# Performance work log

Measured on AMD Instinct MI355X. Metric: run time of the kernel, lower is better.

Reference implementation:

```python
import jax, jax.numpy as jnp
import numpy as np

N_NODES = 200000
N_EDGES = 6400000
D_FEAT = 128
N_CLASSES = 40


def setup_inputs() -> dict:
    key = jax.random.key(0)
    ks = jax.random.split(key, 10)
    s_in = 1.0 / np.sqrt(D_FEAT)
    return {
        "x": jax.random.normal(ks[0], (N_NODES, D_FEAT), dtype=jnp.float32),
        "edge_index": jax.random.randint(ks[1], (2, N_EDGES), 0, N_NODES, dtype=jnp.int64),
        "W0": jax.random.normal(ks[2], (D_FEAT, D_FEAT), dtype=jnp.float32) * s_in,
        "b0": jnp.zeros((D_FEAT,), dtype=jnp.float32),
        "W1": jax.random.normal(ks[3], (D_FEAT, D_FEAT), dtype=jnp.float32) * s_in,
        "b1": jnp.zeros((D_FEAT,), dtype=jnp.float32),
        "W2": jax.random.normal(ks[4], (D_FEAT, D_FEAT), dtype=jnp.float32) * s_in,
        "b2": jnp.zeros((D_FEAT,), dtype=jnp.float32),
        "W3": jax.random.normal(ks[5], (D_FEAT, N_CLASSES), dtype=jnp.float32) * s_in,
        "b3": jnp.zeros((N_CLASSES,), dtype=jnp.float32),
    }


def _silu(h):
    return h * jax.nn.sigmoid(h)


def reference(x, edge_index, W0, b0, W1, b1, W2, b2, W3, b3):
    # PyG ChebConv with K=1: out = Tx_0 @ weight[0] + bias, Tx_0 = x.
    # edge_index feeds the scaled-Laplacian norm, which is unused when K == 1.
    del edge_index
    h = _silu(x @ W0 + b0)            # [N, D] ChebConv + SiLU
    h = _silu(h @ W1 + b1)            # [N, D]
    h = _silu(h @ W2 + b2)            # [N, D]
    logits = h @ W3 + b3              # [N, C]
    return jax.nn.log_softmax(logits, axis=1)
```

## Files before the change

kernel.cpp:

```cpp
#include <hip/hip_runtime.h>

#define NN 200000
#define NW 12
#define NBLK 256
#define NT 12500
#define WSTRIDE (NBLK * NW)

typedef __attribute__((ext_vector_type(8))) short bf16x8;
typedef __attribute__((ext_vector_type(4))) float f32x4;
typedef __attribute__((ext_vector_type(4))) unsigned int u32x4;

static __device__ __forceinline__ short f2bf(float f) {
    unsigned u = __builtin_bit_cast(unsigned, f);
    u += 0x7fffu + ((u >> 16) & 1u);
    return (short)(u >> 16);
}

static __device__ __forceinline__ unsigned pk2(float a, float b) {
    unsigned ua = __builtin_bit_cast(unsigned, a) + 0x8000u;
    unsigned ub = __builtin_bit_cast(unsigned, b) + 0x8000u;
    return __builtin_amdgcn_perm(ub, ua, 0x07060302u);
}

static __device__ __forceinline__ int swz(int r, int k) {
    return (r << 7) + (((k >> 3) ^ (r & 15)) << 3) + (k & 7);
}

__global__ void prep_weights_k(const float* __restrict__ W0, const float* __restrict__ W1,
                               const float* __restrict__ W2, const float* __restrict__ W3,
                               short* __restrict__ wt) {
    int e = blockIdx.x * 256 + threadIdx.x;
    if (e < 49152) {
        int l = e >> 14;
        int i = e & 16383;
        int n = i >> 7, k = i & 127;
        const float* W = (l == 0) ? W0 : ((l == 1) ? W1 : W2);
        wt[e] = f2bf(W[(k << 7) + n]);
    } else if (e < 55296) {
        int i = e - 49152;
        int n = i >> 7, k = i & 127;
        wt[e] = (n < 40) ? f2bf(W3[k * 40 + n]) : (short)0;
    }
}

__global__ __launch_bounds__(768) __attribute__((amdgpu_waves_per_eu(3, 3)))
void mlp_fused_k(const float* __restrict__ x, const short* __restrict__ wt,
                 const float* __restrict__ b0, const float* __restrict__ b1,
                 const float* __restrict__ b2, const float* __restrict__ b3,
                 float* __restrict__ out) {
    __shared__ __align__(16) short sW[55296];
    __shared__ __align__(16) short sA[NW][2048];
    __shared__ __align__(16) float sB[384];

    const int tid  = (int)threadIdx.x;
    const int lane = tid & 63;
    const int wv   = tid >> 6;
    const int m    = lane & 15;
    const int quad = lane >> 4;
    short* sAw = &sA[wv][0];

    {
        const u32x4* src = (const u32x4*)wt;
        #pragma unroll
        for (int i = 0; i < 9; ++i) {
            int q = tid + i * 768;
            int R = q >> 4, c = q & 15;
            *(u32x4*)&sW[(R << 7) + ((c ^ (R & 15)) << 3)] = src[q];
        }
        if (tid < 384)
            sB[tid] = (tid < 128) ? b0[tid] : (tid < 256) ? b1[tid - 128] : b2[tid - 256];
    }
    __syncthreads();

    const bool val2 = (m < 8);
    const float b3v0 = b3[m], b3v1 = b3[16 + m], b3v2 = val2 ? b3[32 + m] : 0.f;

    f32x4 acc[8];
    auto zacc = [&]() {
        #pragma unroll
        for (int ct = 0; ct < 8; ++ct)
            #pragma unroll
            for (int r = 0; r < 4; ++r) acc[ct][r] = 0.f;
    };

    auto epilogue = [&](int lyr) {
        float bb[8];
        #pragma unroll
        for (int ct = 0; ct < 8; ++ct) bb[ct] = sB[(lyr << 7) + (ct << 4) + m];
        #pragma unroll
        for (int ct = 0; ct < 8; ++ct)
            #pragma unroll
            for (int r = 0; r < 4; ++r) {
                float v = acc[ct][r] + bb[ct];
                float h = v * __builtin_amdgcn_rcpf(1.f + __expf(-v));
                int rl = (quad << 2) + r;
                unsigned u = __builtin_bit_cast(unsigned, h) + 0x8000u;
                sAw[swz(rl, (ct << 4) + m)] = (short)(u >> 16);
            }
    };

    auto dense = [&](int lbase) {
        zacc();
        __builtin_amdgcn_s_setprio(1);
        #pragma unroll
        for (int ks = 0; ks < 4; ++ks) {
            int kk = (ks << 5) + (quad << 3);
            bf16x8 a0 = *(const bf16x8*)&sAw[swz(m, kk)];
            #pragma unroll
            for (int ct = 0; ct < 8; ++ct) {
                bf16x8 b = *(const bf16x8*)&sW[lbase + swz((ct << 4) + m, kk)];
                acc[ct] = __builtin_amdgcn_mfma_f32_16x16x32_bf16(a0, b, acc[ct], 0, 0, 0);
            }
        }
        __builtin_amdgcn_s_setprio(0);
    };

    int t = (int)blockIdx.x * NW + wv;
    f32x4 raw[8];
    {
        const f32x4* p = (const f32x4*)(x + ((long)(t * 16 + m) << 7)) + quad * 2;
        #pragma unroll
        for (int ks = 0; ks < 4; ++ks) { raw[ks * 2] = p[ks * 8]; raw[ks * 2 + 1] = p[ks * 8 + 1]; }
    }

    while (true) {
        u32x4 xp[4];
        #pragma unroll
        for (int ks = 0; ks < 4; ++ks) {
            f32x4 va = raw[ks * 2], vb = raw[ks * 2 + 1];
            u32x4 ua;
            ua[0] = pk2(va[0], va[1]); ua[1] = pk2(va[2], va[3]);
            ua[2] = pk2(vb[0], vb[1]); ua[3] = pk2(vb[2], vb[3]);
            xp[ks] = ua;
        }

        zacc();
        __builtin_amdgcn_s_setprio(1);
        #pragma unroll
        for (int ks = 0; ks < 4; ++ks) {
            bf16x8 a0 = __builtin_bit_cast(bf16x8, xp[ks]);
            int kk = (ks << 5) + (quad << 3);
            #pragma unroll
            for (int ct = 0; ct < 8; ++ct) {
                bf16x8 b = *(const bf16x8*)&sW[swz((ct << 4) + m, kk)];
                acc[ct] = __builtin_amdgcn_mfma_f32_16x16x32_bf16(a0, b, acc[ct], 0, 0, 0);
            }
        }
        __builtin_amdgcn_s_setprio(0);
        epilogue(0);
        dense(16384);
        epilogue(1);
        dense(32768);
        epilogue(2);

        int tn = t + WSTRIDE;
        bool has = tn < NT;
        if (has) {
            const f32x4* p = (const f32x4*)(x + ((long)(tn * 16 + m) << 7)) + quad * 2;
            #pragma unroll
            for (int ks = 0; ks < 4; ++ks) { raw[ks * 2] = p[ks * 8]; raw[ks * 2 + 1] = p[ks * 8 + 1]; }
        }

        f32x4 c3[3];
        #pragma unroll
        for (int ct = 0; ct < 3; ++ct)
            #pragma unroll
            for (int r = 0; r < 4; ++r) c3[ct][r] = 0.f;
        __builtin_amdgcn_s_setprio(1);
        #pragma unroll
        for (int ks = 0; ks < 4; ++ks) {
            int kk = (ks << 5) + (quad << 3);
            bf16x8 a0 = *(const bf16x8*)&sAw[swz(m, kk)];
            #pragma unroll
            for (int ct = 0; ct < 3; ++ct) {
                bf16x8 b = *(const bf16x8*)&sW[49152 + swz((ct << 4) + m, kk)];
                c3[ct] = __builtin_amdgcn_mfma_f32_16x16x32_bf16(a0, b, c3[ct], 0, 0, 0);
            }
        }
        __builtin_amdgcn_s_setprio(0);
        #pragma unroll
        for (int r = 0; r < 4; ++r) {
            float v0 = c3[0][r] + b3v0;
            float v1 = c3[1][r] + b3v1;
            float v2 = c3[2][r] + b3v2;
            float mx = fmaxf(v0, v1);
            mx = val2 ? fmaxf(mx, v2) : mx;
            #pragma unroll
            for (int s = 1; s < 16; s <<= 1)
                mx = fmaxf(mx, __shfl_xor(mx, s, 64));
            float sm = __expf(v0 - mx) + __expf(v1 - mx) + (val2 ? __expf(v2 - mx) : 0.f);
            #pragma unroll
            for (int s = 1; s < 16; s <<= 1)
                sm += __shfl_xor(sm, s, 64);
            float L = mx + __logf(sm);
            int grow = t * 16 + (quad << 2) + r;
            float* orow = out + (long)grow * 40;
            orow[m]      = v0 - L;
            orow[16 + m] = v1 - L;
            if (val2) orow[32 + m] = v2 - L;
        }

        if (!has) break;
        t = tn;
    }
}

extern "C" void kernel_launch(void* const* d_in, const int* in_sizes, int n_in,
                              void* d_out, int out_size, void* d_ws, size_t ws_size,
                              hipStream_t stream) {
    const float* x   = (const float*)d_in[0];
    const float* W0  = (const float*)d_in[2];
    const float* bb0 = (const float*)d_in[3];
    const float* W1  = (const float*)d_in[4];
    const float* bb1 = (const float*)d_in[5];
    const float* W2  = (const float*)d_in[6];
    const float* bb2 = (const float*)d_in[7];
    const float* W3  = (const float*)d_in[8];
    const float* bb3 = (const float*)d_in[9];
    short* wt  = (short*)d_ws;
    float* out = (float*)d_out;

    hipLaunchKernelGGL(prep_weights_k, dim3(216), dim3(256), 0, stream, W0, W1, W2, W3, wt);
    hipLaunchKernelGGL(mlp_fused_k, dim3(NBLK), dim3(768), 0, stream,
                       x, wt, bb0, bb1, bb2, bb3, out);
}
```

Baseline: 216.6 us.

## Pack biases into padded weight rows and raise waves per block to thirteen

```diff
diff --git a/kernel.cpp b/kernel.cpp
--- a/kernel.cpp
+++ b/kernel.cpp
@@ -1,7 +1,7 @@
 #include <hip/hip_runtime.h>
 
 #define NN 200000
-#define NW 12
+#define NW 13
 #define NBLK 256
 #define NT 12500
 #define WSTRIDE (NBLK * NW)
@@ -28,7 +28,8 @@
 
 __global__ void prep_weights_k(const float* __restrict__ W0, const float* __restrict__ W1,
                                const float* __restrict__ W2, const float* __restrict__ W3,
-                               short* __restrict__ wt) {
+                               const float* __restrict__ b0, const float* __restrict__ b1,
+                               const float* __restrict__ b2, short* __restrict__ wt) {
     int e = blockIdx.x * 256 + threadIdx.x;
     if (e < 49152) {
         int l = e >> 14;
@@ -39,18 +40,27 @@
     } else if (e < 55296) {
         int i = e - 49152;
         int n = i >> 7, k = i & 127;
-        wt[e] = (n < 40) ? f2bf(W3[k * 40 + n]) : (short)0;
-    }
-}
-
-__global__ __launch_bounds__(768) __attribute__((amdgpu_waves_per_eu(3, 3)))
+        short v = 0;
+        if (n < 40) {
+            v = f2bf(W3[k * 40 + n]);
+        } else {
+            int j2 = e - 54272;
+            if (j2 < 768) {
+                int f = j2 >> 1, lyr = f >> 7, c = f & 127;
+                const float* B = (lyr == 0) ? b0 : ((lyr == 1) ? b1 : b2);
+                unsigned u = __builtin_bit_cast(unsigned, B[c]);
+                v = (short)((j2 & 1) ? (u >> 16) : (u & 0xffffu));
+            }
+        }
+        wt[e] = v;
+    }
+}
+
+__global__ __launch_bounds__(832) __attribute__((amdgpu_waves_per_eu(4, 4)))
 void mlp_fused_k(const float* __restrict__ x, const short* __restrict__ wt,
-                 const float* __restrict__ b0, const float* __restrict__ b1,
-                 const float* __restrict__ b2, const float* __restrict__ b3,
-                 float* __restrict__ out) {
+                 const float* __restrict__ b3, float* __restrict__ out) {
     __shared__ __align__(16) short sW[55296];
     __shared__ __align__(16) short sA[NW][2048];
-    __shared__ __align__(16) float sB[384];
 
     const int tid  = (int)threadIdx.x;
     const int lane = tid & 63;
@@ -62,36 +72,37 @@
     {
         const u32x4* src = (const u32x4*)wt;
         #pragma unroll
-        for (int i = 0; i < 9; ++i) {
-            int q = tid + i * 768;
+        for (int i = 0; i < 8; ++i) {
+            int q = tid + i * 832;
             int R = q >> 4, c = q & 15;
             *(u32x4*)&sW[(R << 7) + ((c ^ (R & 15)) << 3)] = src[q];
         }
-        if (tid < 384)
-            sB[tid] = (tid < 128) ? b0[tid] : (tid < 256) ? b1[tid - 128] : b2[tid - 256];
+        if (tid < 256) {
+            int q = 6656 + tid;
+            int R = q >> 4, c = q & 15;
+            *(u32x4*)&sW[(R << 7) + ((c ^ (R & 15)) << 3)] = src[q];
+        }
     }
     __syncthreads();
 
     const bool val2 = (m < 8);
     const float b3v0 = b3[m], b3v1 = b3[16 + m], b3v2 = val2 ? b3[32 + m] : 0.f;
 
+    auto biasld = [&](int lyr, int ct) -> float {
+        int f = (lyr << 7) + (ct << 4) + m;
+        int r = 424 + (f >> 6);
+        int k = (f & 63) << 1;
+        return *(const float*)&sW[swz(r, k)];
+    };
+
     f32x4 acc[8];
-    auto zacc = [&]() {
+
+    auto epilogue = [&]() {
         #pragma unroll
         for (int ct = 0; ct < 8; ++ct)
             #pragma unroll
-            for (int r = 0; r < 4; ++r) acc[ct][r] = 0.f;
-    };
-
-    auto epilogue = [&](int lyr) {
-        float bb[8];
-        #pragma unroll
-        for (int ct = 0; ct < 8; ++ct) bb[ct] = sB[(lyr << 7) + (ct << 4) + m];
-        #pragma unroll
-        for (int ct = 0; ct < 8; ++ct)
-            #pragma unroll
             for (int r = 0; r < 4; ++r) {
-                float v = acc[ct][r] + bb[ct];
+                float v = acc[ct][r];
                 float h = v * __builtin_amdgcn_rcpf(1.f + __expf(-v));
                 int rl = (quad << 2) + r;
                 unsigned u = __builtin_bit_cast(unsigned, h) + 0x8000u;
@@ -99,8 +110,13 @@
             }
     };
 
-    auto dense = [&](int lbase) {
-        zacc();
+    auto dense = [&](int lbase, int lyr) {
+        #pragma unroll
+        for (int ct = 0; ct < 8; ++ct) {
+            float bb = biasld(lyr, ct);
+            #pragma unroll
+            for (int r = 0; r < 4; ++r) acc[ct][r] = bb;
+        }
         __builtin_amdgcn_s_setprio(1);
         #pragma unroll
         for (int ks = 0; ks < 4; ++ks) {
@@ -116,15 +132,12 @@
     };
 
     int t = (int)blockIdx.x * NW + wv;
-    f32x4 raw[8];
+    u32x4 xp[4];
     {
+        f32x4 raw[8];
         const f32x4* p = (const f32x4*)(x + ((long)(t * 16 + m) << 7)) + quad * 2;
         #pragma unroll
         for (int ks = 0; ks < 4; ++ks) { raw[ks * 2] = p[ks * 8]; raw[ks * 2 + 1] = p[ks * 8 + 1]; }
-    }
-
-    while (true) {
-        u32x4 xp[4];
         #pragma unroll
         for (int ks = 0; ks < 4; ++ks) {
             f32x4 va = raw[ks * 2], vb = raw[ks * 2 + 1];
@@ -133,8 +146,15 @@
             ua[2] = pk2(vb[0], vb[1]); ua[3] = pk2(vb[2], vb[3]);
             xp[ks] = ua;
         }
-
-        zacc();
+    }
+
+    while (true) {
+        #pragma unroll
+        for (int ct = 0; ct < 8; ++ct) {
+            float bb = biasld(0, ct);
+            #pragma unroll
+            for (int r = 0; r < 4; ++r) acc[ct][r] = bb;
+        }
         __builtin_amdgcn_s_setprio(1);
         #pragma unroll
         for (int ks = 0; ks < 4; ++ks) {
@@ -147,14 +167,15 @@
             }
         }
         __builtin_amdgcn_s_setprio(0);
-        epilogue(0);
-        dense(16384);
-        epilogue(1);
-        dense(32768);
-        epilogue(2);
+        epilogue();
+        dense(16384, 1);
+        epilogue();
+        dense(32768, 2);
+        epilogue();
 
         int tn = t + WSTRIDE;
         bool has = tn < NT;
+        f32x4 raw[8];
         if (has) {
             const f32x4* p = (const f32x4*)(x + ((long)(tn * 16 + m) << 7)) + quad * 2;
             #pragma unroll
@@ -163,9 +184,7 @@
 
         f32x4 c3[3];
         #pragma unroll
-        for (int ct = 0; ct < 3; ++ct)
-            #pragma unroll
-            for (int r = 0; r < 4; ++r) c3[ct][r] = 0.f;
+        for (int r = 0; r < 4; ++r) { c3[0][r] = b3v0; c3[1][r] = b3v1; c3[2][r] = b3v2; }
         __builtin_amdgcn_s_setprio(1);
         #pragma unroll
         for (int ks = 0; ks < 4; ++ks) {
@@ -176,13 +195,21 @@
                 bf16x8 b = *(const bf16x8*)&sW[49152 + swz((ct << 4) + m, kk)];
                 c3[ct] = __builtin_amdgcn_mfma_f32_16x16x32_bf16(a0, b, c3[ct], 0, 0, 0);
             }
+            if (has) {
+                f32x4 va = raw[ks * 2], vb = raw[ks * 2 + 1];
+                u32x4 ua;
+                ua[0] = pk2(va[0], va[1]); ua[1] = pk2(va[2], va[3]);
+                ua[2] = pk2(vb[0], vb[1]); ua[3] = pk2(vb[2], vb[3]);
+                xp[ks] = ua;
+            }
         }
         __builtin_amdgcn_s_setprio(0);
+
         #pragma unroll
         for (int r = 0; r < 4; ++r) {
-            float v0 = c3[0][r] + b3v0;
-            float v1 = c3[1][r] + b3v1;
-            float v2 = c3[2][r] + b3v2;
+            float v0 = c3[0][r];
+            float v1 = c3[1][r];
+            float v2 = c3[2][r];
             float mx = fmaxf(v0, v1);
             mx = val2 ? fmaxf(mx, v2) : mx;
             #pragma unroll
@@ -220,7 +247,8 @@
     short* wt  = (short*)d_ws;
     float* out = (float*)d_out;
 
-    hipLaunchKernelGGL(prep_weights_k, dim3(216), dim3(256), 0, stream, W0, W1, W2, W3, wt);
-    hipLaunchKernelGGL(mlp_fused_k, dim3(NBLK), dim3(768), 0, stream,
-                       x, wt, bb0, bb1, bb2, bb3, out);
-}
+    hipLaunchKernelGGL(prep_weights_k, dim3(216), dim3(256), 0, stream,
+                       W0, W1, W2, W3, bb0, bb1, bb2, wt);
+    hipLaunchKernelGGL(mlp_fused_k, dim3(NBLK), dim3(832), 0, stream,
+                       x, wt, bb3, out);
+}
```

Result: slower. 283.8 us (+31.0%).

## Interleave SiLU epilogue with next layer's MFMA k-steps via double accumulators

Applied to the files above, without the earlier changes.

```diff
diff --git a/kernel.cpp b/kernel.cpp
--- a/kernel.cpp
+++ b/kernel.cpp
@@ -75,42 +75,48 @@
     const bool val2 = (m < 8);
     const float b3v0 = b3[m], b3v1 = b3[16 + m], b3v2 = val2 ? b3[32 + m] : 0.f;
 
-    f32x4 acc[8];
-    auto zacc = [&]() {
-        #pragma unroll
-        for (int ct = 0; ct < 8; ++ct)
-            #pragma unroll
-            for (int r = 0; r < 4; ++r) acc[ct][r] = 0.f;
-    };
-
-    auto epilogue = [&](int lyr) {
-        float bb[8];
-        #pragma unroll
-        for (int ct = 0; ct < 8; ++ct) bb[ct] = sB[(lyr << 7) + (ct << 4) + m];
-        #pragma unroll
-        for (int ct = 0; ct < 8; ++ct)
-            #pragma unroll
-            for (int r = 0; r < 4; ++r) {
-                float v = acc[ct][r] + bb[ct];
-                float h = v * __builtin_amdgcn_rcpf(1.f + __expf(-v));
-                int rl = (quad << 2) + r;
-                unsigned u = __builtin_bit_cast(unsigned, h) + 0x8000u;
-                sAw[swz(rl, (ct << 4) + m)] = (short)(u >> 16);
-            }
-    };
-
-    auto dense = [&](int lbase) {
-        zacc();
+    f32x4 accA[8], accB[8];
+
+    auto initb = [&](f32x4* a, int lyr) {
+        #pragma unroll
+        for (int ct = 0; ct < 8; ++ct) {
+            float bb = sB[(lyr << 7) + (ct << 4) + m];
+            #pragma unroll
+            for (int r = 0; r < 4; ++r) a[ct][r] = bb;
+        }
+    };
+
+    auto epi_ct = [&](const f32x4* a, int ct) {
+        #pragma unroll
+        for (int r = 0; r < 4; ++r) {
+            float v = a[ct][r];
+            float h = v * __builtin_amdgcn_rcpf(1.f + __expf(-v));
+            int rl = (quad << 2) + r;
+            unsigned u = __builtin_bit_cast(unsigned, h) + 0x8000u;
+            sAw[swz(rl, (ct << 4) + m)] = (short)(u >> 16);
+        }
+    };
+
+    auto dense_ks = [&](f32x4* a, int lbase, int ks) {
+        int kk = (ks << 5) + (quad << 3);
+        bf16x8 a0 = *(const bf16x8*)&sAw[swz(m, kk)];
         __builtin_amdgcn_s_setprio(1);
         #pragma unroll
-        for (int ks = 0; ks < 4; ++ks) {
-            int kk = (ks << 5) + (quad << 3);
-            bf16x8 a0 = *(const bf16x8*)&sAw[swz(m, kk)];
-            #pragma unroll
-            for (int ct = 0; ct < 8; ++ct) {
-                bf16x8 b = *(const bf16x8*)&sW[lbase + swz((ct << 4) + m, kk)];
-                acc[ct] = __builtin_amdgcn_mfma_f32_16x16x32_bf16(a0, b, acc[ct], 0, 0, 0);
-            }
+        for (int ct = 0; ct < 8; ++ct) {
+            bf16x8 b = *(const bf16x8*)&sW[lbase + swz((ct << 4) + m, kk)];
+            a[ct] = __builtin_amdgcn_mfma_f32_16x16x32_bf16(a0, b, a[ct], 0, 0, 0);
+        }
+        __builtin_amdgcn_s_setprio(0);
+    };
+
+    auto l3_ks = [&](f32x4* c3, int ks) {
+        int kk = (ks << 5) + (quad << 3);
+        bf16x8 a0 = *(const bf16x8*)&sAw[swz(m, kk)];
+        __builtin_amdgcn_s_setprio(1);
+        #pragma unroll
+        for (int ct = 0; ct < 3; ++ct) {
+            bf16x8 b = *(const bf16x8*)&sW[49152 + swz((ct << 4) + m, kk)];
+            c3[ct] = __builtin_amdgcn_mfma_f32_16x16x32_bf16(a0, b, c3[ct], 0, 0, 0);
         }
         __builtin_amdgcn_s_setprio(0);
     };
@@ -134,7 +140,7 @@
             xp[ks] = ua;
         }
 
-        zacc();
+        initb(accA, 0);
         __builtin_amdgcn_s_setprio(1);
         #pragma unroll
         for (int ks = 0; ks < 4; ++ks) {
@@ -143,46 +149,56 @@
             #pragma unroll
             for (int ct = 0; ct < 8; ++ct) {
                 bf16x8 b = *(const bf16x8*)&sW[swz((ct << 4) + m, kk)];
-                acc[ct] = __builtin_amdgcn_mfma_f32_16x16x32_bf16(a0, b, acc[ct], 0, 0, 0);
+                accA[ct] = __builtin_amdgcn_mfma_f32_16x16x32_bf16(a0, b, accA[ct], 0, 0, 0);
             }
         }
         __builtin_amdgcn_s_setprio(0);
-        epilogue(0);
-        dense(16384);
-        epilogue(1);
-        dense(32768);
-        epilogue(2);
+
+        initb(accB, 1);
+        #pragma unroll
+        for (int ks = 0; ks < 4; ++ks) {
+            epi_ct(accA, 2 * ks);
+            epi_ct(accA, 2 * ks + 1);
+            dense_ks(accB, 16384, ks);
+        }
+
+        initb(accA, 2);
+        #pragma unroll
+        for (int ks = 0; ks < 4; ++ks) {
+            epi_ct(accB, 2 * ks);
+            epi_ct(accB, 2 * ks + 1);
+            dense_ks(accA, 32768, ks);
+        }
 
         int tn = t + WSTRIDE;
         bool has = tn < NT;
+
+        f32x4 c3[3];
+        #pragma unroll
+        for (int r = 0; r < 4; ++r) { c3[0][r] = b3v0; c3[1][r] = b3v1; c3[2][r] = b3v2; }
+        #pragma unroll
+        for (int ks = 0; ks < 2; ++ks) {
+            epi_ct(accA, 2 * ks);
+            epi_ct(accA, 2 * ks + 1);
+            l3_ks(c3, ks);
+        }
         if (has) {
             const f32x4* p = (const f32x4*)(x + ((long)(tn * 16 + m) << 7)) + quad * 2;
             #pragma unroll
             for (int ks = 0; ks < 4; ++ks) { raw[ks * 2] = p[ks * 8]; raw[ks * 2 + 1] = p[ks * 8 + 1]; }
         }
-
-        f32x4 c3[3];
-        #pragma unroll
-        for (int ct = 0; ct < 3; ++ct)
-            #pragma unroll
-            for (int r = 0; r < 4; ++r) c3[ct][r] = 0.f;
-        __builtin_amdgcn_s_setprio(1);
-        #pragma unroll
-        for (int ks = 0; ks < 4; ++ks) {
-            int kk = (ks << 5) + (quad << 3);
-            bf16x8 a0 = *(const bf16x8*)&sAw[swz(m, kk)];
-            #pragma unroll
-            for (int ct = 0; ct < 3; ++ct) {
-                bf16x8 b = *(const bf16x8*)&sW[49152 + swz((ct << 4) + m, kk)];
-                c3[ct] = __builtin_amdgcn_mfma_f32_16x16x32_bf16(a0, b, c3[ct], 0, 0, 0);
-            }
-        }
-        __builtin_amdgcn_s_setprio(0);
+        #pragma unroll
+        for (int ks = 2; ks < 4; ++ks) {
+            epi_ct(accA, 2 * ks);
+            epi_ct(accA, 2 * ks + 1);
+            l3_ks(c3, ks);
+        }
+
         #pragma unroll
         for (int r = 0; r < 4; ++r) {
-            float v0 = c3[0][r] + b3v0;
-            float v1 = c3[1][r] + b3v1;
-            float v2 = c3[2][r] + b3v2;
+            float v0 = c3[0][r];
+            float v1 = c3[1][r];
+            float v2 = c3[2][r];
             float mx = fmaxf(v0, v1);
             mx = val2 ? fmaxf(mx, v2) : mx;
             #pragma unroll
```

Measured after the change: 271.3 us. 25.2% more time.
